# Optimization experiments

Measured on AMD Instinct MI355X. Metric: run time of the kernel, lower is better.

Reference implementation:

```python
import jax, jax.numpy as jnp
import numpy as np

N = 262144
HID = 200


def _lin_init(k, out_d, in_d):
    k1, k2 = jax.random.split(k)
    bound = 1.0 / np.sqrt(in_d)
    W = jax.random.uniform(k1, (out_d, in_d), minval=-bound, maxval=bound, dtype=jnp.float32)
    b = jax.random.uniform(k2, (out_d,), minval=-bound, maxval=bound, dtype=jnp.float32)
    return W, b


def setup_inputs() -> dict:
    key = jax.random.key(0)
    ks = jax.random.split(key, 10)
    Wu0, bu0 = _lin_init(ks[0], HID, 3)
    Wu1, bu1 = _lin_init(ks[1], HID, HID)
    Wu2, bu2 = _lin_init(ks[2], 1, HID)
    Wv0, bv0 = _lin_init(ks[3], HID, 3)
    Wv1, bv1 = _lin_init(ks[4], HID, HID)
    Wv2, bv2 = _lin_init(ks[5], 1, HID)
    Wf0, bf0 = _lin_init(ks[6], HID, 12)
    Wf1, bf1 = _lin_init(ks[7], HID, HID)
    Wf2, bf2 = _lin_init(ks[8], 2, HID)
    inputs = jax.random.normal(ks[9], (N, 3), dtype=jnp.float32)
    return dict(inputs=inputs,
                Wu0=Wu0, bu0=bu0, Wu1=Wu1, bu1=bu1, Wu2=Wu2, bu2=bu2,
                Wv0=Wv0, bv0=bv0, Wv1=Wv1, bv1=bv1, Wv2=Wv2, bv2=bv2,
                Wf0=Wf0, bf0=bf0, Wf1=Wf1, bf1=bf1, Wf2=Wf2, bf2=bf2)


def _mlp(x, W0, b0, W1, b1, W2, b2):
    # NN with num_layers=3: sin(Linear) -> sin(Linear) -> Linear
    h = jnp.sin(x @ W0.T + b0)
    h = jnp.sin(h @ W1.T + b1)
    return h @ W2.T + b2


def _scalar(pt, params):
    # per-point scalar network, pt: [3]
    W0, b0, W1, b1, W2, b2 = params
    h = jnp.sin(W0 @ pt + b0)
    h = jnp.sin(W1 @ h + b1)
    return (W2 @ h + b2)[0]


def _derivs(pt, params):
    # first derivatives (grad) and diagonal second derivatives u_xx, u_yy
    # via forward-over-reverse (jvp of grad) with unit tangents e_x, e_y.
    g = jax.grad(lambda p: _scalar(p, params))
    ex = jnp.array([1.0, 0.0, 0.0], dtype=pt.dtype)
    ey = jnp.array([0.0, 1.0, 0.0], dtype=pt.dtype)
    grad, hx = jax.jvp(g, (pt,), (ex,))
    _, hy = jax.jvp(g, (pt,), (ey,))
    return grad, hx[0], hy[1]


def _dhpm_forward(inputs, pu, pv, pf):
    u = _mlp(inputs, *pu)  # [N,1]
    v = _mlp(inputs, *pv)  # [N,1]
    gu, u_xx, u_yy = jax.vmap(lambda p: _derivs(p, pu))(inputs)
    gv, v_xx, v_yy = jax.vmap(lambda p: _derivs(p, pv))(inputs)
    u_x, u_y, u_t = gu[:, :1], gu[:, 1:2], gu[:, 2:3]
    v_x, v_y, v_t = gv[:, :1], gv[:, 1:2], gv[:, 2:3]
    u_xx = u_xx[:, None]; u_yy = u_yy[:, None]
    v_xx = v_xx[:, None]; v_yy = v_yy[:, None]
    feat = jnp.concatenate([u, v, u_t, v_t, u_x, u_xx, u_y, u_yy,
                            v_x, v_xx, v_y, v_yy], axis=1)  # [N,12]
    f = _mlp(feat, *pf)  # [N,2]
    return (u, v, u_t, v_t, u_x, u_xx, u_y, u_yy,
            v_x, v_xx, v_y, v_yy, f[:, :1], f[:, 1:])


def reference(inputs, Wu0, bu0, Wu1, bu1, Wu2, bu2,
              Wv0, bv0, Wv1, bv1, Wv2, bv2,
              Wf0, bf0, Wf1, bf1, Wf2, bf2):
    pu = (Wu0, bu0, Wu1, bu1, Wu2, bu2)
    pv = (Wv0, bv0, Wv1, bv1, Wv2, bv2)
    pf = (Wf0, bf0, Wf1, bf1, Wf2, bf2)
    return _dhpm_forward(inputs, pu, pv, pf)
```

## Files before the change

### kernel.cpp

```cpp
#include <hip/hip_runtime.h>


#define HID 200
#define NT 13
#define KT 7
#define BLDK 232
#define WCHUNK 8192
#define NTH 256

#define OFF_WU 0
#define OFF_WV 106496
#define OFF_WF 212992
#define OFF_CU 319488
#define OFF_CV 322688
#define OFF_CF 325888

typedef _Float16 f16;
typedef _Float16 f16x2 __attribute__((ext_vector_type(2)));
typedef _Float16 f16x8 __attribute__((ext_vector_type(8)));
typedef float f32x4 __attribute__((ext_vector_type(4)));

#define GLDS16(gp, lp) __builtin_amdgcn_global_load_lds( \
    (const __attribute__((address_space(1))) void*)(gp), \
    (__attribute__((address_space(3))) void*)(lp), 16, 0, 0)

__global__ __launch_bounds__(256) void dhpm_prep(
    const float* __restrict__ Wu1, const float* __restrict__ Wv1, const float* __restrict__ Wf1,
    const float* __restrict__ Wu0, const float* __restrict__ bu0,
    const float* __restrict__ Wv0, const float* __restrict__ bv0,
    const float* __restrict__ Wf0, const float* __restrict__ bf0,
    char* __restrict__ ws)
{
    int id = blockIdx.x * blockDim.x + threadIdx.x;
    const int nW = 3 * NT * 16 * 116;
    if (id < nW) {
        const int net = id / (NT*16*116);
        int e = id - net * (NT*16*116);
        const int nt  = e / (16*116);  e -= nt * (16*116);
        const int row = e / 116;
        const int k2  = e - row * 116;
        const int j   = nt*16 + row;
        const int k   = k2*2;
        const float* W = (net == 0) ? Wu1 : (net == 1) ? Wv1 : Wf1;
        f16x2 v; v[0] = (f16)0.f; v[1] = (f16)0.f;
        if (j < HID) {
            if (k     < HID) v[0] = (f16)W[j*HID + k];
            if (k + 1 < HID) v[1] = (f16)W[j*HID + k + 1];
        }
        *(f16x2*)(ws + net*106496 + nt*WCHUNK + row*464 + k2*4) = v;
        return;
    }
    id -= nW;
    if (id < 400) {
        const int net = id / HID;
        const int r   = id - net*HID;
        const float* W0 = net ? Wv0 : Wu0;
        const float* b0 = net ? bv0 : bu0;
        float4 c;
        c.x = W0[r*3+0]; c.y = W0[r*3+1]; c.z = W0[r*3+2]; c.w = b0[r];
        *(float4*)(ws + (net ? OFF_CV : OFF_CU) + r*16) = c;
        return;
    }
    id -= 400;
    if (id < HID) {
        const int i = id;
        float4 c0, c1, c2, c3;
        c0.x = Wf0[i*12+0];  c0.y = Wf0[i*12+1];  c0.z = Wf0[i*12+2];  c0.w = Wf0[i*12+3];
        c1.x = Wf0[i*12+4];  c1.y = Wf0[i*12+5];  c1.z = Wf0[i*12+6];  c1.w = Wf0[i*12+7];
        c2.x = Wf0[i*12+8];  c2.y = Wf0[i*12+9];  c2.z = Wf0[i*12+10]; c2.w = Wf0[i*12+11];
        c3.x = bf0[i]; c3.y = 0.f; c3.z = 0.f; c3.w = 0.f;
        char* p = ws + OFF_CF + i*64;
        *(float4*)(p)      = c0;
        *(float4*)(p + 16) = c1;
        *(float4*)(p + 32) = c2;
        *(float4*)(p + 48) = c3;
    }
}

__device__ __forceinline__ f32x4 mfma16(f16x8 a, f16x8 b, f32x4 c) {
    return __builtin_amdgcn_mfma_f32_16x16x32_f16(a, b, c, 0, 0, 0);
}

__device__ __forceinline__ void run_net(
    const float* __restrict__ inp, const char* __restrict__ ws,
    const int wOff, const int cstOff,
    const float* __restrict__ b1, const float* __restrict__ W2, const float b2s,
    const int cV, const int cXX, const int cYY,
    const int cX, const int cY, const int cT,
    char* __restrict__ Bb0, char* __restrict__ Bb1, float* __restrict__ res,
    const int gp0, const int o, const int lane, const int w,
    const int jl, const int klo)
{
    const char* src = ws + wOff;

    for (int c = w; c < 8; c += 4)
        GLDS16(src + c*1024 + lane*16, Bb0 + c*1024);

    f16x8 aP[6][KT];
    {
        const float4* cst = (const float4*)(ws + cstOff);
        const int pt = gp0 + o + jl;
        const float x = inp[pt*3+0], y = inp[pt*3+1], tt = inp[pt*3+2];
        #pragma unroll
        for (int kt = 0; kt < KT; ++kt) {
            f16x8 f0, f1, f2, f3, f4, f5;
            #pragma unroll
            for (int e = 0; e < 8; ++e) {
                const int i = kt*32 + klo*8 + e;
                const float4 c = cst[(i < HID) ? i : 0];
                const float z = fmaf(c.x, x, fmaf(c.y, y, fmaf(c.z, tt, c.w)));
                float s, cv;
                __sincosf(z, &s, &cv);
                f0[e] = (f16)s;
                f1[e] = (f16)(-s * c.x * c.x);
                f2[e] = (f16)(-s * c.y * c.y);
                f3[e] = (f16)(cv * c.x);
                f4[e] = (f16)(cv * c.y);
                f5[e] = (f16)(cv * c.z);
            }
            aP[0][kt] = f0; aP[1][kt] = f1; aP[2][kt] = f2;
            aP[3][kt] = f3; aP[4][kt] = f4; aP[5][kt] = f5;
        }
    }

    float pV[4]  = {0,0,0,0}, pXX[4] = {0,0,0,0}, pYY[4] = {0,0,0,0};
    float pX[4]  = {0,0,0,0}, pY[4]  = {0,0,0,0}, pT[4]  = {0,0,0,0};

    __syncthreads();

    auto step = [&](const char* Bcur, char* Bnext, const int nt, const int ntNext) {
        if (ntNext < NT)
            for (int c = w; c < 8; c += 4)
                GLDS16(src + ntNext*WCHUNK + c*1024 + lane*16, Bnext + c*1024);

        const f16* BH = (const f16*)Bcur;
        f32x4 acc[6];
        #pragma unroll
        for (int c6 = 0; c6 < 6; ++c6) { f32x4 z = {0.f,0.f,0.f,0.f}; acc[c6] = z; }
        #pragma unroll
        for (int kt = 0; kt < KT; ++kt) {
            const f16x8 b = *(const f16x8*)&BH[jl*BLDK + kt*32 + klo*8];
            #pragma unroll
            for (int c6 = 0; c6 < 6; ++c6)
                acc[c6] = mfma16(aP[c6][kt], b, acc[c6]);
        }

        const int j = nt*16 + jl;
        const float b1j = (j < HID) ? b1[j] : 0.f;
        const float w2j = (j < HID) ? W2[j] : 0.f;
        #pragma unroll
        for (int r = 0; r < 4; ++r) {
            float s1, c1;
            __sincosf(acc[0][r] + b1j, &s1, &c1);
            const float wc = w2j*c1, wsn = w2j*s1;
            const float ydx = acc[3][r], ydy = acc[4][r];
            pV[r]  += wsn;
            pXX[r] = fmaf(wc, acc[1][r], fmaf(-wsn*ydx, ydx, pXX[r]));
            pYY[r] = fmaf(wc, acc[2][r], fmaf(-wsn*ydy, ydy, pYY[r]));
            pX[r]  = fmaf(wc, ydx, pX[r]);
            pY[r]  = fmaf(wc, ydy, pY[r]);
            pT[r]  = fmaf(wc, acc[5][r], pT[r]);
        }
        __syncthreads();
    };

    #pragma unroll
    for (int p2 = 0; p2 < 6; ++p2) {
        step(Bb0, Bb1, 2*p2,     2*p2 + 1);
        step(Bb1, Bb0, 2*p2 + 1, 2*p2 + 2);
    }
    step(Bb0, Bb1, 12, NT);

    #pragma unroll
    for (int d = 1; d < 16; d <<= 1)
        #pragma unroll
        for (int r = 0; r < 4; ++r) {
            pV[r]  += __shfl_xor(pV[r],  d);
            pXX[r] += __shfl_xor(pXX[r], d);
            pYY[r] += __shfl_xor(pYY[r], d);
            pX[r]  += __shfl_xor(pX[r],  d);
            pY[r]  += __shfl_xor(pY[r],  d);
            pT[r]  += __shfl_xor(pT[r],  d);
        }
    if (jl == 0) {
        const int p0 = o + klo*4;
        f32x4 v;
        #pragma unroll
        for (int r = 0; r < 4; ++r) v[r] = pV[r] + b2s;
        *(f32x4*)&res[cV*72 + p0] = v;
        #pragma unroll
        for (int r = 0; r < 4; ++r) v[r] = pXX[r];
        *(f32x4*)&res[cXX*72 + p0] = v;
        #pragma unroll
        for (int r = 0; r < 4; ++r) v[r] = pYY[r];
        *(f32x4*)&res[cYY*72 + p0] = v;
        #pragma unroll
        for (int r = 0; r < 4; ++r) v[r] = pX[r];
        *(f32x4*)&res[cX*72 + p0] = v;
        #pragma unroll
        for (int r = 0; r < 4; ++r) v[r] = pY[r];
        *(f32x4*)&res[cY*72 + p0] = v;
        #pragma unroll
        for (int r = 0; r < 4; ++r) v[r] = pT[r];
        *(f32x4*)&res[cT*72 + p0] = v;
    }
}

__global__ __launch_bounds__(NTH, 2) void dhpm_main(
    const float* __restrict__ inp, const char* __restrict__ ws,
    const float* __restrict__ bu1, const float* __restrict__ Wu2, const float* __restrict__ bu2,
    const float* __restrict__ bv1, const float* __restrict__ Wv2, const float* __restrict__ bv2,
    const float* __restrict__ bf1, const float* __restrict__ Wf2, const float* __restrict__ bf2,
    float* __restrict__ out, const int Np)
{
    __shared__ __align__(16) char LDS[35776];
    char*  Bb0 = LDS;
    char*  Bb1 = LDS + WCHUNK;
    f16*   Af  = (f16*)LDS;
    float* res = (float*)(LDS + 29696);
    float* pfb = (float*)(LDS + 33728);

    const int t = threadIdx.x;
    const int lane = t & 63;
    const int w = __builtin_amdgcn_readfirstlane(t >> 6);
    const int jl = lane & 15, klo = lane >> 4;
    const int o = w * 16;
    const int gp0 = blockIdx.x * 64;

    run_net(inp, ws, OFF_WU, OFF_CU, bu1, Wu2, bu2[0], 0, 5, 7, 4, 6, 2,
            Bb0, Bb1, res, gp0, o, lane, w, jl, klo);
    run_net(inp, ws, OFF_WV, OFF_CV, bv1, Wv2, bv2[0], 1, 9, 11, 8, 10, 3,
            Bb0, Bb1, res, gp0, o, lane, w, jl, klo);

    const int nown = (w == 0) ? 4 : 3;
    f16x8 bF[4][KT];
    #pragma unroll
    for (int ont = 0; ont < 4; ++ont)
        if (ont < nown) {
            const int nt = w + ont*4;
            #pragma unroll
            for (int kt = 0; kt < KT; ++kt)
                bF[ont][kt] = *(const f16x8*)(ws + OFF_WF + nt*WCHUNK
                                              + jl*464 + kt*64 + klo*16);
        }

    {
        float fv[12];
        #pragma unroll
        for (int k = 0; k < 12; ++k) fv[k] = res[k*72 + o + jl];
        const float4* cf = (const float4*)(ws + OFF_CF);
        #pragma unroll
        for (int kt = 0; kt < KT; ++kt) {
            f16x8 f;
            #pragma unroll
            for (int e = 0; e < 8; ++e) {
                const int i = kt*32 + klo*8 + e;
                const int ic = (i < HID) ? i : 0;
                const float4 c0 = cf[ic*4+0];
                const float4 c1 = cf[ic*4+1];
                const float4 c2 = cf[ic*4+2];
                const float4 c3 = cf[ic*4+3];
                float z = c3.x;
                z = fmaf(c0.x, fv[0], z);  z = fmaf(c0.y, fv[1], z);
                z = fmaf(c0.z, fv[2], z);  z = fmaf(c0.w, fv[3], z);
                z = fmaf(c1.x, fv[4], z);  z = fmaf(c1.y, fv[5], z);
                z = fmaf(c1.z, fv[6], z);  z = fmaf(c1.w, fv[7], z);
                z = fmaf(c2.x, fv[8], z);  z = fmaf(c2.y, fv[9], z);
                z = fmaf(c2.z, fv[10], z); z = fmaf(c2.w, fv[11], z);
                f[e] = (f16)__sinf(z);
            }
            *(f16x8*)((char*)Af + (o + jl)*464 + kt*64 + klo*16) = f;
        }
    }
    __syncthreads();

    f32x4 accF[4][4];
    #pragma unroll
    for (int ont = 0; ont < 4; ++ont)
        #pragma unroll
        for (int mt = 0; mt < 4; ++mt) { f32x4 z = {0.f,0.f,0.f,0.f}; accF[ont][mt] = z; }

    #pragma unroll
    for (int kt = 0; kt < KT; ++kt)
        #pragma unroll
        for (int mt = 0; mt < 4; ++mt) {
            const f16x8 a = *(const f16x8*)((const char*)Af
                                + (mt*16 + jl)*464 + kt*64 + klo*16);
            #pragma unroll
            for (int ont = 0; ont < 4; ++ont)
                if (ont < nown)
                    accF[ont][mt] = mfma16(a, bF[ont][kt], accF[ont][mt]);
        }

    float pf0[4][4], pf1[4][4];
    #pragma unroll
    for (int mt = 0; mt < 4; ++mt)
        #pragma unroll
        for (int r = 0; r < 4; ++r) { pf0[mt][r] = 0.f; pf1[mt][r] = 0.f; }

    #pragma unroll
    for (int ont = 0; ont < 4; ++ont)
        if (ont < nown) {
            const int j = (w + ont*4)*16 + jl;
            const float bj = (j < HID) ? bf1[j] : 0.f;
            const float wa = (j < HID) ? Wf2[j] : 0.f;
            const float wb = (j < HID) ? Wf2[HID + j] : 0.f;
            #pragma unroll
            for (int mt = 0; mt < 4; ++mt)
                #pragma unroll
                for (int r = 0; r < 4; ++r) {
                    const float h = __sinf(accF[ont][mt][r] + bj);
                    pf0[mt][r] = fmaf(wa, h, pf0[mt][r]);
                    pf1[mt][r] = fmaf(wb, h, pf1[mt][r]);
                }
        }

    #pragma unroll
    for (int d = 1; d < 16; d <<= 1)
        #pragma unroll
        for (int mt = 0; mt < 4; ++mt)
            #pragma unroll
            for (int r = 0; r < 4; ++r) {
                pf0[mt][r] += __shfl_xor(pf0[mt][r], d);
                pf1[mt][r] += __shfl_xor(pf1[mt][r], d);
            }
    if (jl == 0) {
        #pragma unroll
        for (int mt = 0; mt < 4; ++mt) {
            f32x4 v0, v1;
            #pragma unroll
            for (int r = 0; r < 4; ++r) { v0[r] = pf0[mt][r]; v1[r] = pf1[mt][r]; }
            *(f32x4*)&pfb[w*128 + 0*64 + mt*16 + klo*4] = v0;
            *(f32x4*)&pfb[w*128 + 1*64 + mt*16 + klo*4] = v1;
        }
    }
    __syncthreads();
    if (t < 128) {
        const int pt = t & 63, ch = t >> 6;
        float s = bf2[ch];
        #pragma unroll
        for (int ww = 0; ww < 4; ++ww) s += pfb[ww*128 + ch*64 + pt];
        res[(12 + ch)*72 + pt] = s;
    }
    __syncthreads();

    for (int e = t; e < 14*64; e += NTH) {
        const int c = e >> 6, p = e & 63;
        out[(size_t)c*Np + gp0 + p] = res[c*72 + p];
    }
}

extern "C" void kernel_launch(void* const* d_in, const int* in_sizes, int n_in,
                              void* d_out, int out_size, void* d_ws, size_t ws_size,
                              hipStream_t stream) {
    const float* inp = (const float*)d_in[0];
    const float* Wu0 = (const float*)d_in[1];  const float* bu0 = (const float*)d_in[2];
    const float* Wu1 = (const float*)d_in[3];  const float* bu1 = (const float*)d_in[4];
    const float* Wu2 = (const float*)d_in[5];  const float* bu2 = (const float*)d_in[6];
    const float* Wv0 = (const float*)d_in[7];  const float* bv0 = (const float*)d_in[8];
    const float* Wv1 = (const float*)d_in[9];  const float* bv1 = (const float*)d_in[10];
    const float* Wv2 = (const float*)d_in[11]; const float* bv2 = (const float*)d_in[12];
    const float* Wf0 = (const float*)d_in[13]; const float* bf0 = (const float*)d_in[14];
    const float* Wf1 = (const float*)d_in[15]; const float* bf1 = (const float*)d_in[16];
    const float* Wf2 = (const float*)d_in[17]; const float* bf2 = (const float*)d_in[18];
    float* out = (float*)d_out;
    char* ws = (char*)d_ws;

    const int Np = in_sizes[0] / 3;

    const int nTot = 3*NT*16*116 + 400 + HID;
    dhpm_prep<<<(nTot + NTH - 1) / NTH, NTH, 0, stream>>>(
        Wu1, Wv1, Wf1, Wu0, bu0, Wv0, bv0, Wf0, bf0, ws);
    dhpm_main<<<Np / 64, NTH, 0, stream>>>(
        inp, ws, bu1, Wu2, bu2, bv1, Wv2, bv2, bf1, Wf2, bf2, out, Np);
}
```

Before: 757.9 us.

## Split each point tile across two waves for sin and cos derivative paths

Doubles the block to 8 waves. Each 16-point tile is now handled by a pair of waves: one builds the sin-based A-fragments (value and second derivatives), the other the cos-based ones (first derivatives). The pair swaps intermediate values through an LDS exchange buffer, with an extra barrier per N-tile. This halves per-wave A-fragment and accumulator registers so more waves fit per CU, and spreads the f-network tiles over 8 waves. The cost is additional LDS traffic and a second __syncthreads in every inner step.

```diff
diff --git a/kernel.cpp b/kernel.cpp
--- a/kernel.cpp
+++ b/kernel.cpp
@@ -6,7 +6,8 @@
 #define KT 7
 #define BLDK 232
 #define WCHUNK 8192
-#define NTH 256
+#define NTH 512
+#define ELD 68
 
 #define OFF_WU 0
 #define OFF_WV 106496
@@ -87,122 +88,143 @@
     const float* __restrict__ b1, const float* __restrict__ W2, const float b2s,
     const int cV, const int cXX, const int cYY,
     const int cX, const int cY, const int cT,
-    char* __restrict__ Bb0, char* __restrict__ Bb1, float* __restrict__ res,
-    const int gp0, const int o, const int lane, const int w,
+    char* __restrict__ Bb0, char* __restrict__ Bb1,
+    float* __restrict__ exch, float* __restrict__ res,
+    const int gp0, const int lane, const int w, const int q, const int g,
     const int jl, const int klo)
 {
     const char* src = ws + wOff;
 
-    for (int c = w; c < 8; c += 4)
-        GLDS16(src + c*1024 + lane*16, Bb0 + c*1024);
-
-    f16x8 aP[6][KT];
+    GLDS16(src + w*1024 + lane*16, Bb0 + w*1024);
+
+    f16x8 aP[3][KT];
     {
         const float4* cst = (const float4*)(ws + cstOff);
-        const int pt = gp0 + o + jl;
+        const int pt = gp0 + q*16 + jl;
         const float x = inp[pt*3+0], y = inp[pt*3+1], tt = inp[pt*3+2];
         #pragma unroll
         for (int kt = 0; kt < KT; ++kt) {
-            f16x8 f0, f1, f2, f3, f4, f5;
+            f16x8 f0, f1, f2;
             #pragma unroll
             for (int e = 0; e < 8; ++e) {
                 const int i = kt*32 + klo*8 + e;
                 const float4 c = cst[(i < HID) ? i : 0];
                 const float z = fmaf(c.x, x, fmaf(c.y, y, fmaf(c.z, tt, c.w)));
-                float s, cv;
-                __sincosf(z, &s, &cv);
-                f0[e] = (f16)s;
-                f1[e] = (f16)(-s * c.x * c.x);
-                f2[e] = (f16)(-s * c.y * c.y);
-                f3[e] = (f16)(cv * c.x);
-                f4[e] = (f16)(cv * c.y);
-                f5[e] = (f16)(cv * c.z);
+                if (g == 0) {
+                    const float s = __sinf(z);
+                    f0[e] = (f16)s;
+                    f1[e] = (f16)(-s * c.x * c.x);
+                    f2[e] = (f16)(-s * c.y * c.y);
+                } else {
+                    const float cv = __cosf(z);
+                    f0[e] = (f16)(cv * c.x);
+                    f1[e] = (f16)(cv * c.y);
+                    f2[e] = (f16)(cv * c.z);
+                }
             }
             aP[0][kt] = f0; aP[1][kt] = f1; aP[2][kt] = f2;
-            aP[3][kt] = f3; aP[4][kt] = f4; aP[5][kt] = f5;
-        }
-    }
-
-    float pV[4]  = {0,0,0,0}, pXX[4] = {0,0,0,0}, pYY[4] = {0,0,0,0};
-    float pX[4]  = {0,0,0,0}, pY[4]  = {0,0,0,0}, pT[4]  = {0,0,0,0};
+        }
+    }
+
+    float p0a[4] = {0,0,0,0}, p1a[4] = {0,0,0,0}, p2a[4] = {0,0,0,0};
+
+    float* E0  = exch;
+    float* Edx = exch + 16*ELD;
+    float* Edy = exch + 32*ELD;
 
     __syncthreads();
 
-    auto step = [&](const char* Bcur, char* Bnext, const int nt, const int ntNext) {
-        if (ntNext < NT)
-            for (int c = w; c < 8; c += 4)
-                GLDS16(src + ntNext*WCHUNK + c*1024 + lane*16, Bnext + c*1024);
-
+    for (int nt = 0; nt < NT; ++nt) {
+        const char* Bcur = (nt & 1) ? Bb1 : Bb0;
+        char*       Bnxt = (nt & 1) ? Bb0 : Bb1;
+        if (nt + 1 < NT)
+            GLDS16(src + (nt+1)*WCHUNK + w*1024 + lane*16, Bnxt + w*1024);
+
+        f32x4 acc0 = {0,0,0,0}, acc1 = {0,0,0,0}, acc2 = {0,0,0,0};
         const f16* BH = (const f16*)Bcur;
-        f32x4 acc[6];
-        #pragma unroll
-        for (int c6 = 0; c6 < 6; ++c6) { f32x4 z = {0.f,0.f,0.f,0.f}; acc[c6] = z; }
         #pragma unroll
         for (int kt = 0; kt < KT; ++kt) {
             const f16x8 b = *(const f16x8*)&BH[jl*BLDK + kt*32 + klo*8];
-            #pragma unroll
-            for (int c6 = 0; c6 < 6; ++c6)
-                acc[c6] = mfma16(aP[c6][kt], b, acc[c6]);
+            acc0 = mfma16(aP[0][kt], b, acc0);
+            acc1 = mfma16(aP[1][kt], b, acc1);
+            acc2 = mfma16(aP[2][kt], b, acc2);
         }
 
         const int j = nt*16 + jl;
         const float b1j = (j < HID) ? b1[j] : 0.f;
         const float w2j = (j < HID) ? W2[j] : 0.f;
+        const int pcol = q*16 + klo*4;
+        float wcr[4], wsr[4];
+        if (g == 0) {
+            f32x4 wc4;
+            #pragma unroll
+            for (int r = 0; r < 4; ++r) {
+                float s1, c1;
+                __sincosf(acc0[r] + b1j, &s1, &c1);
+                wcr[r] = w2j * c1;
+                wsr[r] = w2j * s1;
+                p0a[r] += wsr[r];
+                wc4[r] = wcr[r];
+            }
+            *(f32x4*)&E0[jl*ELD + pcol] = wc4;
+        } else {
+            *(f32x4*)&Edx[jl*ELD + pcol] = acc0;
+            *(f32x4*)&Edy[jl*ELD + pcol] = acc1;
+        }
+        __syncthreads();
+
+        if (g == 0) {
+            const f32x4 ydx = *(const f32x4*)&Edx[jl*ELD + pcol];
+            const f32x4 ydy = *(const f32x4*)&Edy[jl*ELD + pcol];
+            #pragma unroll
+            for (int r = 0; r < 4; ++r) {
+                p1a[r] = fmaf(wcr[r], acc1[r], fmaf(-wsr[r]*ydx[r], ydx[r], p1a[r]));
+                p2a[r] = fmaf(wcr[r], acc2[r], fmaf(-wsr[r]*ydy[r], ydy[r], p2a[r]));
+            }
+        } else {
+            const f32x4 wc4 = *(const f32x4*)&E0[jl*ELD + pcol];
+            #pragma unroll
+            for (int r = 0; r < 4; ++r) {
+                p0a[r] = fmaf(wc4[r], acc0[r], p0a[r]);
+                p1a[r] = fmaf(wc4[r], acc1[r], p1a[r]);
+                p2a[r] = fmaf(wc4[r], acc2[r], p2a[r]);
+            }
+        }
+        __syncthreads();
+    }
+
+    #pragma unroll
+    for (int d = 1; d < 16; d <<= 1)
         #pragma unroll
         for (int r = 0; r < 4; ++r) {
-            float s1, c1;
-            __sincosf(acc[0][r] + b1j, &s1, &c1);
-            const float wc = w2j*c1, wsn = w2j*s1;
-            const float ydx = acc[3][r], ydy = acc[4][r];
-            pV[r]  += wsn;
-            pXX[r] = fmaf(wc, acc[1][r], fmaf(-wsn*ydx, ydx, pXX[r]));
-            pYY[r] = fmaf(wc, acc[2][r], fmaf(-wsn*ydy, ydy, pYY[r]));
-            pX[r]  = fmaf(wc, ydx, pX[r]);
-            pY[r]  = fmaf(wc, ydy, pY[r]);
-            pT[r]  = fmaf(wc, acc[5][r], pT[r]);
-        }
-        __syncthreads();
-    };
-
-    #pragma unroll
-    for (int p2 = 0; p2 < 6; ++p2) {
-        step(Bb0, Bb1, 2*p2,     2*p2 + 1);
-        step(Bb1, Bb0, 2*p2 + 1, 2*p2 + 2);
-    }
-    step(Bb0, Bb1, 12, NT);
-
-    #pragma unroll
-    for (int d = 1; d < 16; d <<= 1)
-        #pragma unroll
-        for (int r = 0; r < 4; ++r) {
-            pV[r]  += __shfl_xor(pV[r],  d);
-            pXX[r] += __shfl_xor(pXX[r], d);
-            pYY[r] += __shfl_xor(pYY[r], d);
-            pX[r]  += __shfl_xor(pX[r],  d);
-            pY[r]  += __shfl_xor(pY[r],  d);
-            pT[r]  += __shfl_xor(pT[r],  d);
+            p0a[r] += __shfl_xor(p0a[r], d);
+            p1a[r] += __shfl_xor(p1a[r], d);
+            p2a[r] += __shfl_xor(p2a[r], d);
         }
     if (jl == 0) {
-        const int p0 = o + klo*4;
+        const int p0 = q*16 + klo*4;
         f32x4 v;
-        #pragma unroll
-        for (int r = 0; r < 4; ++r) v[r] = pV[r] + b2s;
-        *(f32x4*)&res[cV*72 + p0] = v;
-        #pragma unroll
-        for (int r = 0; r < 4; ++r) v[r] = pXX[r];
-        *(f32x4*)&res[cXX*72 + p0] = v;
-        #pragma unroll
-        for (int r = 0; r < 4; ++r) v[r] = pYY[r];
-        *(f32x4*)&res[cYY*72 + p0] = v;
-        #pragma unroll
-        for (int r = 0; r < 4; ++r) v[r] = pX[r];
-        *(f32x4*)&res[cX*72 + p0] = v;
-        #pragma unroll
-        for (int r = 0; r < 4; ++r) v[r] = pY[r];
-        *(f32x4*)&res[cY*72 + p0] = v;
-        #pragma unroll
-        for (int r = 0; r < 4; ++r) v[r] = pT[r];
-        *(f32x4*)&res[cT*72 + p0] = v;
+        if (g == 0) {
+            #pragma unroll
+            for (int r = 0; r < 4; ++r) v[r] = p0a[r] + b2s;
+            *(f32x4*)&res[cV*72 + p0] = v;
+            #pragma unroll
+            for (int r = 0; r < 4; ++r) v[r] = p1a[r];
+            *(f32x4*)&res[cXX*72 + p0] = v;
+            #pragma unroll
+            for (int r = 0; r < 4; ++r) v[r] = p2a[r];
+            *(f32x4*)&res[cYY*72 + p0] = v;
+        } else {
+            #pragma unroll
+            for (int r = 0; r < 4; ++r) v[r] = p0a[r];
+            *(f32x4*)&res[cX*72 + p0] = v;
+            #pragma unroll
+            for (int r = 0; r < 4; ++r) v[r] = p1a[r];
+            *(f32x4*)&res[cY*72 + p0] = v;
+            #pragma unroll
+            for (int r = 0; r < 4; ++r) v[r] = p2a[r];
+            *(f32x4*)&res[cT*72 + p0] = v;
+        }
     }
 }
 
@@ -213,41 +235,45 @@
     const float* __restrict__ bf1, const float* __restrict__ Wf2, const float* __restrict__ bf2,
     float* __restrict__ out, const int Np)
 {
-    __shared__ __align__(16) char LDS[35776];
-    char*  Bb0 = LDS;
-    char*  Bb1 = LDS + WCHUNK;
-    f16*   Af  = (f16*)LDS;
-    float* res = (float*)(LDS + 29696);
-    float* pfb = (float*)(LDS + 33728);
+    __shared__ __align__(16) char LDS[37824];
+    char*  Bb0  = LDS;
+    char*  Bb1  = LDS + 8192;
+    float* exch = (float*)(LDS + 16384);
+    f16*   Af   = (f16*)LDS;
+    float* res  = (float*)(LDS + 29696);
+    float* pfb  = (float*)(LDS + 33728);
 
     const int t = threadIdx.x;
     const int lane = t & 63;
     const int w = __builtin_amdgcn_readfirstlane(t >> 6);
+    const int q = w & 3, g = w >> 2;
     const int jl = lane & 15, klo = lane >> 4;
-    const int o = w * 16;
     const int gp0 = blockIdx.x * 64;
 
     run_net(inp, ws, OFF_WU, OFF_CU, bu1, Wu2, bu2[0], 0, 5, 7, 4, 6, 2,
-            Bb0, Bb1, res, gp0, o, lane, w, jl, klo);
+            Bb0, Bb1, exch, res, gp0, lane, w, q, g, jl, klo);
     run_net(inp, ws, OFF_WV, OFF_CV, bv1, Wv2, bv2[0], 1, 9, 11, 8, 10, 3,
-            Bb0, Bb1, res, gp0, o, lane, w, jl, klo);
-
-    const int nown = (w == 0) ? 4 : 3;
-    f16x8 bF[4][KT];
-    #pragma unroll
-    for (int ont = 0; ont < 4; ++ont)
+            Bb0, Bb1, exch, res, gp0, lane, w, q, g, jl, klo);
+
+    __syncthreads();
+
+    const int nown = (w < 5) ? 2 : 1;
+    f16x8 bF[2][KT];
+    #pragma unroll
+    for (int ont = 0; ont < 2; ++ont)
         if (ont < nown) {
-            const int nt = w + ont*4;
+            const int nt = w + ont*8;
             #pragma unroll
             for (int kt = 0; kt < KT; ++kt)
                 bF[ont][kt] = *(const f16x8*)(ws + OFF_WF + nt*WCHUNK
                                               + jl*464 + kt*64 + klo*16);
         }
 
-    {
+    if (w < 4) {
+        const int p = w*16 + jl;
         float fv[12];
         #pragma unroll
-        for (int k = 0; k < 12; ++k) fv[k] = res[k*72 + o + jl];
+        for (int k = 0; k < 12; ++k) fv[k] = res[k*72 + p];
         const float4* cf = (const float4*)(ws + OFF_CF);
         #pragma unroll
         for (int kt = 0; kt < KT; ++kt) {
@@ -269,16 +295,16 @@
                 z = fmaf(c2.z, fv[10], z); z = fmaf(c2.w, fv[11], z);
                 f[e] = (f16)__sinf(z);
             }
-            *(f16x8*)((char*)Af + (o + jl)*464 + kt*64 + klo*16) = f;
+            *(f16x8*)((char*)Af + p*464 + kt*64 + klo*16) = f;
         }
     }
     __syncthreads();
 
-    f32x4 accF[4][4];
-    #pragma unroll
-    for (int ont = 0; ont < 4; ++ont)
-        #pragma unroll
-        for (int mt = 0; mt < 4; ++mt) { f32x4 z = {0.f,0.f,0.f,0.f}; accF[ont][mt] = z; }
+    f32x4 accF[2][4];
+    #pragma unroll
+    for (int ont = 0; ont < 2; ++ont)
+        #pragma unroll
+        for (int mt = 0; mt < 4; ++mt) { f32x4 z = {0,0,0,0}; accF[ont][mt] = z; }
 
     #pragma unroll
     for (int kt = 0; kt < KT; ++kt)
@@ -287,7 +313,7 @@
             const f16x8 a = *(const f16x8*)((const char*)Af
                                 + (mt*16 + jl)*464 + kt*64 + klo*16);
             #pragma unroll
-            for (int ont = 0; ont < 4; ++ont)
+            for (int ont = 0; ont < 2; ++ont)
                 if (ont < nown)
                     accF[ont][mt] = mfma16(a, bF[ont][kt], accF[ont][mt]);
         }
@@ -299,9 +325,9 @@
         for (int r = 0; r < 4; ++r) { pf0[mt][r] = 0.f; pf1[mt][r] = 0.f; }
 
     #pragma unroll
-    for (int ont = 0; ont < 4; ++ont)
+    for (int ont = 0; ont < 2; ++ont)
         if (ont < nown) {
-            const int j = (w + ont*4)*16 + jl;
+            const int j = (w + ont*8)*16 + jl;
             const float bj = (j < HID) ? bf1[j] : 0.f;
             const float wa = (j < HID) ? Wf2[j] : 0.f;
             const float wb = (j < HID) ? Wf2[HID + j] : 0.f;
@@ -339,7 +365,7 @@
         const int pt = t & 63, ch = t >> 6;
         float s = bf2[ch];
         #pragma unroll
-        for (int ww = 0; ww < 4; ++ww) s += pfb[ww*128 + ch*64 + pt];
+        for (int ww = 0; ww < 8; ++ww) s += pfb[ww*128 + ch*64 + pt];
         res[(12 + ch)*72 + pt] = s;
     }
     __syncthreads();
@@ -369,7 +395,7 @@
     const int Np = in_sizes[0] / 3;
 
     const int nTot = 3*NT*16*116 + 400 + HID;
-    dhpm_prep<<<(nTot + NTH - 1) / NTH, NTH, 0, stream>>>(
+    dhpm_prep<<<(nTot + 255) / 256, 256, 0, stream>>>(
         Wu1, Wv1, Wf1, Wu0, bu0, Wv0, bv0, Wf0, bf0, ws);
     dhpm_main<<<Np / 64, NTH, 0, stream>>>(
         inp, ws, bu1, Wu2, bu2, bv1, Wv2, bv2, bf1, Wf2, bf2, out, Np);
```

After: 718.3 us. 5.2% less time.
